# Kernel tuning notes

Measured on AMD Instinct MI355X. Metric: run time of the kernel, lower is better.

Reference implementation:

```python
import jax, jax.numpy as jnp
import numpy as np
from jax import lax

ULB_LEN = 50000  # hardcoded ulb_dest_len in Cluster.__init__
EPS = 1e-8       # torch.cosine_similarity eps


def _l2norm(x):
    n = jnp.sqrt(jnp.sum(x * x, axis=-1, keepdims=True))
    return x / jnp.maximum(n, EPS)


def setup_inputs() -> dict:
    key = jax.random.key(0)
    k1, k2, k3, k4, k5 = jax.random.split(key, 5)
    B, C, D, K = 32768, 1000, 256, 16
    return {
        "feature": jax.random.normal(k1, (B, D), dtype=jnp.float32),
        "pred": jax.random.normal(k2, (B, C), dtype=jnp.float32),
        "centroids": jax.random.normal(k3, (C, D), dtype=jnp.float32),
        "pred_top_N": jax.random.uniform(k4, (C, K), dtype=jnp.float32),
        "unlabeled_index": jax.random.randint(k5, (B,), 0, ULB_LEN, dtype=jnp.int64),
    }


def reference(feature, pred, centroids, pred_top_N, unlabeled_index):
    B = feature.shape[0]
    C, K = pred_top_N.shape

    # batched cosine similarity to centroids -> argmax label, max cos
    cos = _l2norm(feature) @ _l2norm(centroids).T          # [B, C]
    label = jnp.argmax(cos, axis=1)                        # [B]
    cos_f = jnp.max(cos, axis=1)                           # [B]

    # confidence scores from softmax(pred)
    scores = jnp.max(jax.nn.softmax(pred, axis=1), axis=1)  # [B]

    # per-class mean / unbiased variance of cos_f (torch.var default unbiased)
    ones = jnp.ones((B,), dtype=cos_f.dtype)
    cnt = jax.ops.segment_sum(ones, label, num_segments=C)
    s1 = jax.ops.segment_sum(cos_f, label, num_segments=C)
    s2 = jax.ops.segment_sum(cos_f * cos_f, label, num_segments=C)
    mean = s1 / jnp.maximum(cnt, 1.0)
    var = (s2 - cnt * mean * mean) / jnp.maximum(cnt - 1.0, 1.0)
    std = jnp.sqrt(jnp.maximum(var, 0.0) + 1e-12)

    # weight[i] = normal(mean, std).pdf(cos_f[i]) if cos_f[i] < mean[label] else 1
    m_i, s_i = mean[label], std[label]
    inv_sqrt_2pi = 1.0 / jnp.sqrt(2.0 * jnp.pi).astype(cos_f.dtype)
    pdf = jnp.exp(-0.5 * ((cos_f - m_i) / s_i) ** 2) * inv_sqrt_2pi / s_i
    weight = jnp.where(cos_f < m_i, pdf, jnp.ones_like(cos_f))

    # sequential top-N scatter-insert into pred_top_N / fake_index
    fake_index = jnp.full((C, K), -1, dtype=jnp.int32)

    def step(carry, xs):
        topN, fidx = carry
        lb, sc, ui = xs
        row = topN[lb]                       # [K]
        mi = jnp.argmin(row)
        mv = row[mi]
        do = sc > mv
        topN = topN.at[lb, mi].set(jnp.where(do, sc, mv))
        fidx = fidx.at[lb, mi].set(jnp.where(do, ui.astype(jnp.int32), fidx[lb, mi]))
        return (topN, fidx), None

    (topN, fidx), _ = lax.scan(
        step, (pred_top_N, fake_index),
        (label, scores, unlabeled_index))

    # selected_label scatter (all samples selected: select==1 everywhere)
    selected_label = jnp.full((ULB_LEN,), -1, dtype=jnp.int32)
    selected_label = selected_label.at[unlabeled_index].set(label.astype(jnp.int32))

    return label.astype(jnp.float32), weight, topN, fidx, selected_label
```

## Files before the change

### kernel.cpp

```cpp
#include <hip/hip_runtime.h>
#include <cstdint>
#include <cstddef>

#define B_N   32768
#define C_N   1000
#define C_PAD 1024
#define D_N   256
#define K_N   16
#define ULB_N 50000
#define NCHUNK 128
#define CAP_L 128

#define OFF_L 0
#define OFF_W 32768
#define OFF_T 65536
#define OFF_F 81536
#define OFF_S 97536

typedef __attribute__((ext_vector_type(8))) short short8;
typedef __attribute__((ext_vector_type(4))) float f32x4;

__device__ __forceinline__ unsigned ordf(float f) {
  unsigned u = __float_as_uint(f);
  return (u & 0x80000000u) ? ~u : (u | 0x80000000u);
}
__device__ __forceinline__ float iordf(unsigned h) {
  unsigned u = (h & 0x80000000u) ? (h & 0x7FFFFFFFu) : ~h;
  return __uint_as_float(u);
}
__device__ __forceinline__ unsigned short f2bf(float f) {
  unsigned u = __float_as_uint(f);
  return (unsigned short)((u + 0x7FFFu + ((u >> 16) & 1u)) >> 16);
}
__device__ __forceinline__ float bf2f(unsigned short h) {
  return __uint_as_float(((unsigned)h) << 16);
}

__device__ __forceinline__ void pack_body(const float* __restrict__ src,
                                          short8* __restrict__ dst,
                                          int mtL, int mt0, int nreal) {
  __shared__ float s[16][260];
  __shared__ float part[16][16];
  __shared__ float dv[16];
  const int t = threadIdx.x;
  const int r = t >> 4, c4 = (t & 15) * 4;
  const int grow = (mt0 + mtL) * 16 + r;
  #pragma unroll
  for (int i = 0; i < 4; ++i) {
    float4 v;
    if (grow < nreal) v = *reinterpret_cast<const float4*>(&src[(size_t)grow * D_N + c4 + 64 * i]);
    else { v.x = 0.f; v.y = 0.f; v.z = 0.f; v.w = 0.f; }
    s[r][c4 + 64 * i + 0] = v.x; s[r][c4 + 64 * i + 1] = v.y;
    s[r][c4 + 64 * i + 2] = v.z; s[r][c4 + 64 * i + 3] = v.w;
  }
  __syncthreads();
  {
    int c0 = t & 15;
    float ss = 0.f;
    #pragma unroll
    for (int j = 0; j < 16; ++j) { float x = s[r][c0 + 16 * j]; ss += x * x; }
    part[r][c0] = ss;
  }
  __syncthreads();
  if (t < 16) {
    float ss = 0.f;
    #pragma unroll
    for (int j = 0; j < 16; ++j) ss += part[t][j];
    dv[t] = 1.0f / fmaxf(sqrtf(ss), 1e-8f);
  }
  __syncthreads();
  #pragma unroll
  for (int i = 0; i < 4; ++i) {
    int p = t + 256 * i;
    int si = p >> 6, l = p & 63;
    int mr = l & 15, g = l >> 4;
    int kc = (si & 7) * 32 + g * 8;
    bool lo = si >= 8;
    float di = dv[mr];
    short8 v;
    #pragma unroll
    for (int j = 0; j < 8; ++j) {
      float q = s[mr][kc + j] * di;
      unsigned short hi = f2bf(q);
      unsigned short e = lo ? f2bf(q - bf2f(hi)) : hi;
      v[j] = (short)e;
    }
    dst[(size_t)mtL * 1024 + p] = v;
  }
}

__global__ __launch_bounds__(256) void k_initpack(const float* __restrict__ cent,
                                                  short8* __restrict__ Bp,
                                                  unsigned long long* keys, float* s1, float* s2,
                                                  int* cnt, int* besti) {
  int i = blockIdx.x * blockDim.x + threadIdx.x;
  if (i < B_N)  keys[i] = 0ull;
  if (i < C_PAD) { s1[i] = 0.f; s2[i] = 0.f; cnt[i] = 0; }
  if (i < ULB_N) besti[i] = -1;
  if (blockIdx.x < 64) pack_body(cent, Bp, blockIdx.x, 0, C_N);
}

__global__ __launch_bounds__(256) void k_pack(const float* __restrict__ src,
                                              short8* __restrict__ dst,
                                              int mt0, int nreal) {
  pack_body(src, dst, blockIdx.x, mt0, nreal);
}

__global__ __launch_bounds__(256, 2) void k_mfma(const short8* __restrict__ Ap,
                                                 const short8* __restrict__ Bp,
                                                 unsigned long long* __restrict__ keys,
                                                 int row0) {
  const int bid = blockIdx.x;
  const int nby = gridDim.x >> 3;
  int byl, bx;
  if ((nby & 63) == 0) {
    int xcd = bid & 7, j = bid >> 3;
    int slab = nby >> 3;
    int grp = j >> 6, jj = j & 63;
    byl = xcd * slab + grp * 8 + (jj & 7);
    bx = jj >> 3;
  } else { byl = bid >> 3; bx = bid & 7; }

  const int w = threadIdx.x >> 6, l = threadIdx.x & 63;
  const int wm = (w & 1) * 64, wn = (w >> 1) * 64;
  const short8* a0 = Ap + (size_t)(byl * 8 + (wm >> 4)) * 1024 + l;
  const short8* b0 = Bp + (size_t)(bx * 8 + (wn >> 4)) * 1024 + l;

  f32x4 acc[4][4];
  #pragma unroll
  for (int i = 0; i < 4; ++i)
    #pragma unroll
    for (int j = 0; j < 4; ++j) { acc[i][j][0] = 0.f; acc[i][j][1] = 0.f; acc[i][j][2] = 0.f; acc[i][j][3] = 0.f; }

  short8 A0h[4], B0h[4], A0l[4], B0l[4];
  short8 A1h[4], B1h[4], A1l[4], B1l[4];
#define LOADSET(Xh, Yh, Xl, Yl, ks) { \
    _Pragma("unroll") \
    for (int i = 0; i < 4; ++i) Xh[i] = a0[(ks) * 64 + i * 1024]; \
    _Pragma("unroll") \
    for (int i = 0; i < 4; ++i) Yh[i] = b0[(ks) * 64 + i * 1024]; \
    _Pragma("unroll") \
    for (int i = 0; i < 4; ++i) Xl[i] = a0[((ks) + 8) * 64 + i * 1024]; \
    _Pragma("unroll") \
    for (int i = 0; i < 4; ++i) Yl[i] = b0[((ks) + 8) * 64 + i * 1024]; }
#define MFMA16(fa, fb) { \
    _Pragma("unroll") \
    for (int mi = 0; mi < 4; ++mi) \
      _Pragma("unroll") \
      for (int nj = 0; nj < 4; ++nj) \
        acc[mi][nj] = __builtin_amdgcn_mfma_f32_16x16x32_bf16(fa[mi], fb[nj], acc[mi][nj], 0, 0, 0); }
#define MFMA48(Xh, Yh, Xl, Yl) { MFMA16(Xh, Yh) MFMA16(Xl, Yh) MFMA16(Xh, Yl) }

  LOADSET(A0h, B0h, A0l, B0l, 0)
  #pragma unroll 1
  for (int ks = 0; ks < 8; ks += 2) {
    LOADSET(A1h, B1h, A1l, B1l, ks + 1)
    MFMA48(A0h, B0h, A0l, B0l)
    if (ks + 2 < 8) LOADSET(A0h, B0h, A0l, B0l, ks + 2)
    MFMA48(A1h, B1h, A1l, B1l)
  }
#undef LOADSET
#undef MFMA16
#undef MFMA48

  const int cb = bx * 128 + wn + (l & 15);
  #pragma unroll
  for (int mi = 0; mi < 4; ++mi) {
    #pragma unroll
    for (int r = 0; r < 4; ++r) {
      float bv = -INFINITY; int bc = 0x7FFFFFFF;
      #pragma unroll
      for (int nj = 0; nj < 4; ++nj) {
        int c = cb + nj * 16;
        float v = acc[mi][nj][r];
        if (c < C_N && v > bv) { bv = v; bc = c; }
      }
      #pragma unroll
      for (int mk = 1; mk < 16; mk <<= 1) {
        float ov = __shfl_xor(bv, mk, 64);
        int oc = __shfl_xor(bc, mk, 64);
        if (ov > bv || (ov == bv && oc < bc)) { bv = ov; bc = oc; }
      }
      if ((l & 15) == 0) {
        unsigned long long kk =
            (((unsigned long long)ordf(bv)) << 32) |
            (unsigned long long)(0xFFFFFFFFu - (unsigned)bc);
        atomicMax(&keys[row0 + byl * 128 + wm + mi * 16 + (l >> 4) * 4 + r], kk);
      }
    }
  }
}

__global__ __launch_bounds__(256) void k_scores(const float* __restrict__ pred,
                                                float* __restrict__ scores) {
  __shared__ float red[8];
  int r = blockIdx.x, t = threadIdx.x;
  const float* row = pred + (size_t)r * C_N;
  float4 v;
  bool act = t < 250;
  if (act) v = *reinterpret_cast<const float4*>(&row[t * 4]);
  else { v.x = -INFINITY; v.y = -INFINITY; v.z = -INFINITY; v.w = -INFINITY; }
  float m = fmaxf(fmaxf(v.x, v.y), fmaxf(v.z, v.w));
  #pragma unroll
  for (int mk = 1; mk < 64; mk <<= 1) m = fmaxf(m, __shfl_xor(m, mk, 64));
  int wid = t >> 6, lane = t & 63;
  if (lane == 0) red[wid] = m;
  __syncthreads();
  m = fmaxf(fmaxf(red[0], red[1]), fmaxf(red[2], red[3]));
  float s = act ? expf(v.x - m) + expf(v.y - m) + expf(v.z - m) + expf(v.w - m) : 0.f;
  #pragma unroll
  for (int mk = 1; mk < 64; mk <<= 1) s += __shfl_xor(s, mk, 64);
  __syncthreads();
  if (lane == 0) red[4 + wid] = s;
  __syncthreads();
  if (t == 0) {
    float S = ((red[4] + red[5]) + red[6]) + red[7];
    scores[r] = 1.0f / S;
  }
}

__global__ __launch_bounds__(256) void k_post(const unsigned long long* __restrict__ keys,
                                              const int* __restrict__ ui,
                                              int* __restrict__ labels, float* __restrict__ cosf_,
                                              float* __restrict__ s1, float* __restrict__ s2,
                                              int* __restrict__ cnt, int* __restrict__ besti,
                                              unsigned short* __restrict__ lrank,
                                              unsigned short* __restrict__ hist,
                                              float* __restrict__ out) {
  __shared__ int lab[256];
  __shared__ unsigned histl[C_PAD];
  int chunk = blockIdx.x, t = threadIdx.x;
  int b = chunk * 256 + t;
  #pragma unroll
  for (int r = 0; r < 4; ++r) histl[t + 256 * r] = 0;
  unsigned long long k = keys[b];
  int c = (int)(0xFFFFFFFFu - (unsigned)k);
  float f = iordf((unsigned)(k >> 32));
  labels[b] = c;
  cosf_[b] = f;
  out[OFF_L + b] = (float)c;
  atomicAdd(&s1[c], f);
  atomicAdd(&s2[c], f * f);
  atomicAdd(&cnt[c], 1);
  atomicMax(&besti[ui[b]], b);
  lab[t] = c;
  __syncthreads();
  atomicAdd(&histl[c], 1u);
  unsigned rk = 0;
  for (int j = 0; j < t; ++j) rk += (lab[j] == c);
  lrank[b] = (unsigned short)rk;
  __syncthreads();
  #pragma unroll
  for (int r = 0; r < 4; ++r)
    hist[chunk * C_PAD + t + 256 * r] = (unsigned short)histl[t + 256 * r];
}

__global__ void k_prefix(const unsigned short* __restrict__ hist,
                         unsigned short* __restrict__ base,
                         int* __restrict__ class_n) {
  int c = blockIdx.x * 64 + threadIdx.x;
  unsigned run = 0;
  for (int t = 0; t < NCHUNK; ++t) {
    unsigned h = hist[t * C_PAD + c];
    base[t * C_PAD + c] = (unsigned short)run;
    run += h;
  }
  class_n[c] = (int)run;
}

__global__ __launch_bounds__(256) void k_sw(const int* __restrict__ labels,
                                            const unsigned short* __restrict__ lrank,
                                            const unsigned short* __restrict__ base,
                                            const float* __restrict__ scores,
                                            const int* __restrict__ ui,
                                            const float* __restrict__ cosf_,
                                            const float* __restrict__ s1,
                                            const float* __restrict__ s2,
                                            const int* __restrict__ cnt,
                                            const int* __restrict__ besti,
                                            float* __restrict__ lists_s,
                                            int* __restrict__ lists_u,
                                            float* __restrict__ out) {
  int b = blockIdx.x * blockDim.x + threadIdx.x;
  if (b >= B_N) return;
  int c = labels[b];
  int chunk = b >> 8;
  int pos = (int)base[chunk * C_PAD + c] + (int)lrank[b];
  if (pos < CAP_L) {
    lists_s[c * CAP_L + pos] = scores[b];
    lists_u[c * CAP_L + pos] = ui[b];
  }
  float n = (float)cnt[c];
  float m = s1[c] / fmaxf(n, 1.0f);
  float var = (s2[c] - n * m * m) / fmaxf(n - 1.0f, 1.0f);
  float sd = sqrtf(fmaxf(var, 0.0f) + 1e-12f);
  float cf = cosf_[b];
  float wgt = 1.0f;
  if (cf < m) {
    float z = (cf - m) / sd;
    const float inv = 0.3989422804014327f;
    wgt = expf(-0.5f * (z * z)) * inv / sd;
  }
  out[OFF_W + b] = wgt;
  {
    int bi = besti[b];
    out[OFF_S + b] = (bi < 0) ? -1.0f : (float)labels[bi];
  }
  int p2 = b + B_N;
  if (p2 < ULB_N) {
    int bi = besti[p2];
    out[OFF_S + p2] = (bi < 0) ? -1.0f : (float)labels[bi];
  }
}

__global__ __launch_bounds__(256) void k_replay(const float* __restrict__ ptn,
                                                const float* __restrict__ lists_s,
                                                const int* __restrict__ lists_u,
                                                const int* __restrict__ class_n,
                                                const int* __restrict__ labels,
                                                const float* __restrict__ scores,
                                                const int* __restrict__ ui,
                                                float* __restrict__ out) {
  int c = blockIdx.x * 4 + (threadIdx.x >> 6);
  int lane = threadIdx.x & 63;
  if (c >= C_N) return;

  float tv[K_N]; int fi[K_N];
  #pragma unroll
  for (int j = 0; j < K_N; ++j) { tv[j] = ptn[c * K_N + j]; fi[j] = -1; }

  auto ins = [&](float s, int u) {
    float mv = tv[0]; int mi = 0;
    #pragma unroll
    for (int j = 1; j < K_N; ++j) { if (tv[j] < mv) { mv = tv[j]; mi = j; } }
    if (s > mv) {
      #pragma unroll
      for (int j = 0; j < K_N; ++j) { if (j == mi) { tv[j] = s; fi[j] = u; } }
    }
  };

  int n = class_n[c];
  if (n <= CAP_L) {
    for (int t0 = 0; t0 < n; t0 += 64) {
      float s = 0.f; int u = 0;
      int idx = t0 + lane;
      if (idx < n) { s = lists_s[c * CAP_L + idx]; u = lists_u[c * CAP_L + idx]; }
      int lim = min(64, n - t0);
      for (int t = 0; t < lim; ++t) {
        float ss = __shfl(s, t, 64);
        int uu = __shfl(u, t, 64);
        ins(ss, uu);
      }
    }
  } else {
    for (int t0 = 0; t0 < B_N; t0 += 64) {
      int lb = labels[t0 + lane];
      unsigned long long match = __ballot(lb == c);
      while (match) {
        int t = __ffsll((long long)match) - 1;
        match &= match - 1;
        int b = t0 + t;
        ins(scores[b], ui[b]);
      }
    }
  }

  if (lane == 0) {
    #pragma unroll
    for (int j = 0; j < K_N; ++j) {
      out[OFF_T + c * K_N + j] = tv[j];
      out[OFF_F + c * K_N + j] = (float)fi[j];
    }
  }
}

extern "C" void kernel_launch(void* const* d_in, const int* in_sizes, int n_in,
                              void* d_out, int out_size, void* d_ws, size_t ws_size,
                              hipStream_t stream) {
  const float* feat = (const float*)d_in[0];
  const float* pred = (const float*)d_in[1];
  const float* cent = (const float*)d_in[2];
  const float* ptn  = (const float*)d_in[3];
  const int*   ui   = (const int*)d_in[4];
  float* out = (float*)d_out;
  char* ws = (char*)d_ws;

  size_t o = 0;
  auto alloc = [&](size_t bytes) { void* p = ws + o; o += (bytes + 255) & ~size_t(255); return p; };
  short8* Bp                = (short8*)alloc(64 * 1024 * 16);
  unsigned long long* keys  = (unsigned long long*)alloc(B_N * 8);
  int*   labels             = (int*)  alloc(B_N * 4);
  float* scores             = (float*)alloc(B_N * 4);
  float* cosf_              = (float*)alloc(B_N * 4);
  float* s1                 = (float*)alloc(C_PAD * 4);
  float* s2                 = (float*)alloc(C_PAD * 4);
  int*   cnt                = (int*)  alloc(C_PAD * 4);
  int*   besti              = (int*)  alloc(ULB_N * 4);
  unsigned short* lrank     = (unsigned short*)alloc(B_N * 2);
  unsigned short* hist      = (unsigned short*)alloc(NCHUNK * C_PAD * 2);
  unsigned short* base      = (unsigned short*)alloc(NCHUNK * C_PAD * 2);
  int*   class_n            = (int*)  alloc(C_PAD * 4);
  float* lists_s            = (float*)alloc(C_N * CAP_L * 4);
  int*   lists_u            = (int*)  alloc(C_N * CAP_L * 4);

  size_t avail = (ws_size > o) ? ws_size - o : 0;
  int g128 = (int)(avail / 131072ull);
  if (g128 < 1) g128 = 1;
  if (g128 > 256) g128 = 256;
  if (g128 >= 64) g128 &= ~63;
  else if (g128 >= 8) g128 &= ~7;
  short8* Achunk = (short8*)(ws + o);

  k_initpack <<<196, 256, 0, stream>>>(cent, Bp, keys, s1, s2, cnt, besti);
  for (int c0 = 0; c0 < 256; c0 += g128) {
    int g = (g128 < 256 - c0) ? g128 : (256 - c0);
    k_pack   <<<g * 8, 256, 0, stream>>>(feat, Achunk, c0 * 8, B_N);
    k_mfma   <<<g * 8, 256, 0, stream>>>(Achunk, Bp, keys, c0 * 128);
  }
  k_scores   <<<B_N, 256, 0, stream>>>(pred, scores);
  k_post     <<<NCHUNK, 256, 0, stream>>>(keys, ui, labels, cosf_, s1, s2, cnt, besti, lrank, hist, out);
  k_prefix   <<<16, 64, 0, stream>>>(hist, base, class_n);
  k_sw       <<<B_N / 256, 256, 0, stream>>>(labels, lrank, base, scores, ui, cosf_, s1, s2, cnt, besti, lists_s, lists_u, out);
  k_replay   <<<250, 256, 0, stream>>>(ptn, lists_s, lists_u, class_n, labels, scores, ui, out);
}
```

Baseline: 161.9 us.

## Stage MFMA operand tiles through LDS via direct global-to-LDS loads

The bf16 split GEMM kernel used to load A and B fragments straight from global memory into registers for each wave, so waves sharing rows or columns fetched the same data repeatedly. It now stages each k-step's A and B tiles into a double-buffered shared memory buffer with global_load_lds and reads the fragments from LDS. This is meant to cut redundant global and L2 traffic and register pressure. In exchange it adds a __syncthreads per k-step and LDS read latency, and the staged load may not be fully overlapped with compute.

```diff
diff --git a/kernel.cpp b/kernel.cpp
--- a/kernel.cpp
+++ b/kernel.cpp
@@ -110,6 +110,7 @@
                                                  const short8* __restrict__ Bp,
                                                  unsigned long long* __restrict__ keys,
                                                  int row0) {
+  __shared__ short8 sbuf[2][2048];
   const int bid = blockIdx.x;
   const int nby = gridDim.x >> 3;
   int byl, bx;
@@ -123,8 +124,8 @@
 
   const int w = threadIdx.x >> 6, l = threadIdx.x & 63;
   const int wm = (w & 1) * 64, wn = (w >> 1) * 64;
-  const short8* a0 = Ap + (size_t)(byl * 8 + (wm >> 4)) * 1024 + l;
-  const short8* b0 = Bp + (size_t)(bx * 8 + (wn >> 4)) * 1024 + l;
+  const size_t abase = (size_t)(byl * 8) * 1024 + l;
+  const size_t bbase = (size_t)(bx * 8) * 1024 + l;
 
   f32x4 acc[4][4];
   #pragma unroll
@@ -132,36 +133,50 @@
     #pragma unroll
     for (int j = 0; j < 4; ++j) { acc[i][j][0] = 0.f; acc[i][j][1] = 0.f; acc[i][j][2] = 0.f; acc[i][j][3] = 0.f; }
 
-  short8 A0h[4], B0h[4], A0l[4], B0l[4];
-  short8 A1h[4], B1h[4], A1l[4], B1l[4];
-#define LOADSET(Xh, Yh, Xl, Yl, ks) { \
+#define STAGE(buf_, ks_) { \
     _Pragma("unroll") \
-    for (int i = 0; i < 4; ++i) Xh[i] = a0[(ks) * 64 + i * 1024]; \
-    _Pragma("unroll") \
-    for (int i = 0; i < 4; ++i) Yh[i] = b0[(ks) * 64 + i * 1024]; \
-    _Pragma("unroll") \
-    for (int i = 0; i < 4; ++i) Xl[i] = a0[((ks) + 8) * 64 + i * 1024]; \
-    _Pragma("unroll") \
-    for (int i = 0; i < 4; ++i) Yl[i] = b0[((ks) + 8) * 64 + i * 1024]; }
+    for (int i = 0; i < 8; ++i) { \
+      int c = w * 8 + i; \
+      const short8* g; \
+      if (c < 16) g = Ap + abase + (size_t)(c >> 1) * 1024 + (size_t)(((ks_) + (c & 1) * 8) * 64); \
+      else        g = Bp + bbase + (size_t)((c - 16) >> 1) * 1024 + (size_t)(((ks_) + (c & 1) * 8) * 64); \
+      __builtin_amdgcn_global_load_lds( \
+          (const __attribute__((address_space(1))) void*)g, \
+          (__attribute__((address_space(3))) void*)&sbuf[buf_][c * 64], 16, 0, 0); \
+    } }
 #define MFMA16(fa, fb) { \
     _Pragma("unroll") \
     for (int mi = 0; mi < 4; ++mi) \
       _Pragma("unroll") \
       for (int nj = 0; nj < 4; ++nj) \
         acc[mi][nj] = __builtin_amdgcn_mfma_f32_16x16x32_bf16(fa[mi], fb[nj], acc[mi][nj], 0, 0, 0); }
-#define MFMA48(Xh, Yh, Xl, Yl) { MFMA16(Xh, Yh) MFMA16(Xl, Yh) MFMA16(Xh, Yl) }
-
-  LOADSET(A0h, B0h, A0l, B0l, 0)
+
+  const int mtb = (w & 1) * 4;
+  const int ntb = (w >> 1) * 4;
+  short8 Ah[4], Al[4], Bh[4], Bl[4];
+
+  int buf = 0;
+  STAGE(0, 0)
+  __syncthreads();
   #pragma unroll 1
-  for (int ks = 0; ks < 8; ks += 2) {
-    LOADSET(A1h, B1h, A1l, B1l, ks + 1)
-    MFMA48(A0h, B0h, A0l, B0l)
-    if (ks + 2 < 8) LOADSET(A0h, B0h, A0l, B0l, ks + 2)
-    MFMA48(A1h, B1h, A1l, B1l)
-  }
-#undef LOADSET
+  for (int ks = 0; ks < 8; ++ks) {
+    if (ks < 7) STAGE(buf ^ 1, ks + 1)
+    #pragma unroll
+    for (int i = 0; i < 4; ++i) Ah[i] = sbuf[buf][(mtb + i) * 128 + l];
+    #pragma unroll
+    for (int i = 0; i < 4; ++i) Bh[i] = sbuf[buf][1024 + (ntb + i) * 128 + l];
+    #pragma unroll
+    for (int i = 0; i < 4; ++i) Al[i] = sbuf[buf][(mtb + i) * 128 + 64 + l];
+    #pragma unroll
+    for (int i = 0; i < 4; ++i) Bl[i] = sbuf[buf][1024 + (ntb + i) * 128 + 64 + l];
+    MFMA16(Ah, Bh)
+    MFMA16(Al, Bh)
+    MFMA16(Ah, Bl)
+    __syncthreads();
+    buf ^= 1;
+  }
+#undef STAGE
 #undef MFMA16
-#undef MFMA48
 
   const int cb = bx * 128 + wn + (l & 15);
   #pragma unroll
```

Result: no change. 163.3 us (+0.8%).
